# Kernel optimization log

Hardware: AMD Instinct MI355X
Metric: run time of the kernel (lower is better)

The kernel has to match this reference:

```python
import jax, jax.numpy as jnp
import numpy as np

DIM = 1024
D_STATE = 64
D_CONV = 4
EXPAND = 2
D_INNER = DIM * EXPAND          # 2048
N_HEADS = D_INNER // 64         # 32
HEAD_DIM = D_INNER // N_HEADS   # 64
B_SZ = 1
SEQ = 1024
D_IN_PROJ = 2 * D_INNER + 2 * D_STATE + N_HEADS  # 4256
EPS = 1e-6


def setup_inputs() -> dict:
    key = jax.random.key(0)
    ks = jax.random.split(key, 9)
    x = jax.random.normal(ks[0], (B_SZ, SEQ, DIM), jnp.float32)
    W_in = jax.random.normal(ks[1], (D_IN_PROJ, DIM), jnp.float32) / np.sqrt(DIM)
    W_conv = jax.random.normal(ks[2], (D_INNER, 1, D_CONV), jnp.float32) / np.sqrt(D_CONV)
    b_conv = 0.01 * jax.random.normal(ks[3], (D_INNER,), jnp.float32)
    # A_log init: log(arange(1..d_state)) broadcast to (h, d, n), as in the module
    A_log = jnp.log(jnp.arange(1, D_STATE + 1, dtype=jnp.float32)) * jnp.ones((N_HEADS, HEAD_DIM, D_STATE), jnp.float32)
    D = jnp.ones((N_HEADS, HEAD_DIM), jnp.float32) + 0.01 * jax.random.normal(ks[4], (N_HEADS, HEAD_DIM), jnp.float32)
    dt_bias = 0.1 * jax.random.normal(ks[5], (N_HEADS,), jnp.float32)
    norm_w = jnp.ones((D_INNER,), jnp.float32) + 0.01 * jax.random.normal(ks[6], (D_INNER,), jnp.float32)
    W_out = jax.random.normal(ks[7], (DIM, D_INNER), jnp.float32) / np.sqrt(D_INNER)
    return {"x": x, "W_in": W_in, "W_conv": W_conv, "b_conv": b_conv,
            "A_log": A_log, "D": D, "dt_bias": dt_bias, "norm_w": norm_w, "W_out": W_out}


def reference(x, W_in, W_conv, b_conv, A_log, D, dt_bias, norm_w, W_out):
    Bsz, L, _ = x.shape
    zxBCdt = x @ W_in.T  # (B, L, D_IN_PROJ)
    z, xin, Bm, Cm, dt = jnp.split(
        zxBCdt,
        [D_INNER, 2 * D_INNER, 2 * D_INNER + D_STATE, 2 * D_INNER + 2 * D_STATE],
        axis=-1)
    # causal depthwise conv1d (padding d_conv-1 then truncate == left-pad d_conv-1)
    xc = jnp.transpose(xin, (0, 2, 1))  # (B, d_inner, L)
    xc = jax.lax.conv_general_dilated(
        xc, W_conv, window_strides=(1,), padding=[(D_CONV - 1, 0)],
        feature_group_count=D_INNER, dimension_numbers=("NCH", "OIH", "NCH"))
    xc = xc + b_conv[None, :, None]
    xin = jax.nn.silu(jnp.transpose(xc, (0, 2, 1)))  # (B, L, d_inner)
    xh = xin.reshape(Bsz, L, N_HEADS, HEAD_DIM)      # (B, L, h, d)

    A = -jnp.exp(A_log)                     # (h, d, n)
    dt = jax.nn.softplus(dt + dt_bias)      # (B, L, h)

    def step(h_state, ins):
        x_t, dt_t, B_t, C_t = ins  # (B,h,d), (B,h), (B,n), (B,n)
        a = jnp.exp(dt_t[:, :, None, None] * A[None])          # (B,h,d,n)
        h_state = a * h_state + B_t[:, None, None, :] * x_t[..., None]
        y_t = jnp.einsum("bhdn,bn->bhd", h_state, C_t)
        return h_state, y_t

    h0 = jnp.zeros((Bsz, N_HEADS, HEAD_DIM, D_STATE), x.dtype)
    xs = (jnp.moveaxis(xh, 1, 0), jnp.moveaxis(dt, 1, 0),
          jnp.moveaxis(Bm, 1, 0), jnp.moveaxis(Cm, 1, 0))
    _, ys = jax.lax.scan(step, h0, xs)
    y = jnp.moveaxis(ys, 0, 1)              # (B, L, h, d)
    y = y + xh * D[None, None]              # skip term
    y = y.reshape(Bsz, L, D_INNER)
    y = y * jax.nn.silu(z)                  # gating
    rms = jnp.sqrt(jnp.mean(y * y, axis=-1, keepdims=True) + EPS)
    y = y / rms * norm_w                    # RMSNorm
    return y @ W_out.T                      # (B, L, dim)
```

## Files before the change

kernel.cpp:

```cpp
#include <hip/hip_runtime.h>

typedef unsigned short u16;
typedef unsigned int u32;
typedef __attribute__((ext_vector_type(8))) short bf16x8;
typedef __attribute__((ext_vector_type(4))) float f32x4;

#define GPTR(p) ((const __attribute__((address_space(1))) void*)(p))
#define SPTR(p) ((__attribute__((address_space(3))) void*)(p))

#define L_SEQ 1024
#define DIM 1024
#define D_INNER 2048
#define D_STATE 64
#define N_HEADS 32
#define NPROJ 4256
#define NPROJ_PAD 4352
#define COL_Z 0
#define COL_X 2048
#define COL_B 4096
#define COL_C 4160
#define COL_DT 4224
#define NCHUNK 32
#define QCH 32

__device__ __forceinline__ u16 f2bf(float f) {
    unsigned int u = __float_as_uint(f);
    u = u + 0x7fffu + ((u >> 16) & 1u);
    return (u16)(u >> 16);
}
__device__ __forceinline__ float bf2f(u16 h) {
    unsigned int u = ((unsigned int)h) << 16;
    return __uint_as_float(u);
}

__global__ __launch_bounds__(256)
void cast_all_kernel(const float* __restrict__ x, const float* __restrict__ W_in,
                     const float* __restrict__ W_out,
                     u16* __restrict__ xb_hi, u16* __restrict__ xb_lo,
                     u16* __restrict__ Winb, u16* __restrict__ Winb_lo,
                     u16* __restrict__ Woutb)
{
    const int b = blockIdx.x;
    if (b < 1024) {
        const int i = (b * 256 + threadIdx.x) * 4;
        const float4 v = *(const float4*)&x[i];
        const float vs[4] = { v.x, v.y, v.z, v.w };
        u16 oh[4], ol[4];
        #pragma unroll
        for (int j = 0; j < 4; ++j) {
            oh[j] = f2bf(vs[j]);
            ol[j] = f2bf(vs[j] - bf2f(oh[j]));
        }
        *(ushort4*)&xb_hi[i] = *(ushort4*)oh;
        *(ushort4*)&xb_lo[i] = *(ushort4*)ol;
    } else if (b < 5376) {
        const int i = ((b - 1024) * 256 + threadIdx.x) * 4;
        float4 v = make_float4(0.f, 0.f, 0.f, 0.f);
        if (i < NPROJ * DIM) v = *(const float4*)&W_in[i];
        u16 o[4] = { f2bf(v.x), f2bf(v.y), f2bf(v.z), f2bf(v.w) };
        *(ushort4*)&Winb[i] = *(ushort4*)o;
    } else if (b < 5632) {
        const int i = ((b - 5376) * 256 + threadIdx.x) * 4;
        float4 v = make_float4(0.f, 0.f, 0.f, 0.f);
        if (i < (NPROJ - 4096) * DIM) v = *(const float4*)&W_in[(size_t)4096 * DIM + i];
        const float vs[4] = { v.x, v.y, v.z, v.w };
        u16 oh[4], ol[4];
        #pragma unroll
        for (int j = 0; j < 4; ++j) {
            oh[j] = f2bf(vs[j]);
            ol[j] = f2bf(vs[j] - bf2f(oh[j]));
        }
        *(ushort4*)&Winb[(size_t)4096 * DIM + i] = *(ushort4*)oh;
        *(ushort4*)&Winb_lo[i] = *(ushort4*)ol;
    } else {
        const int i = ((b - 5632) * 256 + threadIdx.x) * 4;
        const float4 v = *(const float4*)&W_out[i];
        u16 o[4] = { f2bf(v.x), f2bf(v.y), f2bf(v.z), f2bf(v.w) };
        *(ushort4*)&Woutb[i] = *(ushort4*)o;
    }
}

__global__ __launch_bounds__(256, 2)
void gemm_bt64(const u16* __restrict__ Ah, const u16* __restrict__ Al,
               const u16* __restrict__ Bh, const u16* __restrict__ Bl,
               float* __restrict__ C, int K, int ldc, int precise_from)
{
    __shared__ u16 As[2][64 * 32];
    __shared__ u16 Bs[2][64 * 32];
    __shared__ u16 AsL[2][64 * 32];
    __shared__ u16 BsL[2][64 * 32];
    const int tid  = threadIdx.x;
    const int wave = tid >> 6;
    const int lane = tid & 63;
    const int row0 = blockIdx.y * 64;
    const int col0 = blockIdx.x * 64;
    const int wm = (wave >> 1) * 32;
    const int wn = (wave & 1) * 32;
    const bool precise = ((int)blockIdx.x >= precise_from);

    f32x4 acc[2][2] = {};

    const int r15 = lane & 15;
    const int ko  = (lane >> 4) * 8;

    const int srr = tid >> 2;
    const int skk = (tid & 3) * 8;
    const int lofs = wave * 512;

    auto stage = [&](int buf, int kt) {
        const size_t goff = (size_t)(row0 + srr) * K + kt + skk;
        const size_t gofb = (size_t)(col0 + srr) * K + kt + skk;
        __builtin_amdgcn_global_load_lds(GPTR(Ah + goff), SPTR(&As[buf][lofs]), 16, 0, 0);
        __builtin_amdgcn_global_load_lds(GPTR(Bh + gofb), SPTR(&Bs[buf][lofs]), 16, 0, 0);
        if (precise) {
            __builtin_amdgcn_global_load_lds(GPTR(Al + goff), SPTR(&AsL[buf][lofs]), 16, 0, 0);
            __builtin_amdgcn_global_load_lds(GPTR(Bl + gofb), SPTR(&BsL[buf][lofs]), 16, 0, 0);
        }
    };

    stage(0, 0);
    __syncthreads();
    int cur = 0;
    const int nt = K / 32;
    for (int it = 0; it < nt; ++it) {
        if (it + 1 < nt) stage(cur ^ 1, (it + 1) * 32);
        bf16x8 av[2], bv[2];
        #pragma unroll
        for (int i = 0; i < 2; ++i)
            av[i] = *(const bf16x8*)&As[cur][(wm + i * 16 + r15) * 32 + ko];
        #pragma unroll
        for (int j = 0; j < 2; ++j)
            bv[j] = *(const bf16x8*)&Bs[cur][(wn + j * 16 + r15) * 32 + ko];
        if (precise) {
            bf16x8 avl[2], bvl[2];
            #pragma unroll
            for (int i = 0; i < 2; ++i)
                avl[i] = *(const bf16x8*)&AsL[cur][(wm + i * 16 + r15) * 32 + ko];
            #pragma unroll
            for (int j = 0; j < 2; ++j)
                bvl[j] = *(const bf16x8*)&BsL[cur][(wn + j * 16 + r15) * 32 + ko];
            #pragma unroll
            for (int i = 0; i < 2; ++i)
                #pragma unroll
                for (int j = 0; j < 2; ++j) {
                    acc[i][j] = __builtin_amdgcn_mfma_f32_16x16x32_bf16(av[i],  bv[j],  acc[i][j], 0, 0, 0);
                    acc[i][j] = __builtin_amdgcn_mfma_f32_16x16x32_bf16(av[i],  bvl[j], acc[i][j], 0, 0, 0);
                    acc[i][j] = __builtin_amdgcn_mfma_f32_16x16x32_bf16(avl[i], bv[j],  acc[i][j], 0, 0, 0);
                }
        } else {
            #pragma unroll
            for (int i = 0; i < 2; ++i)
                #pragma unroll
                for (int j = 0; j < 2; ++j)
                    acc[i][j] = __builtin_amdgcn_mfma_f32_16x16x32_bf16(av[i], bv[j], acc[i][j], 0, 0, 0);
        }
        __syncthreads();
        cur ^= 1;
    }

    const int cl = lane & 15;
    const int rg = (lane >> 4) * 4;
    #pragma unroll
    for (int i = 0; i < 2; ++i)
        #pragma unroll
        for (int j = 0; j < 2; ++j)
            #pragma unroll
            for (int reg = 0; reg < 4; ++reg) {
                const int rrow = row0 + wm + i * 16 + rg + reg;
                const int ccol = col0 + wn + j * 16 + cl;
                C[(size_t)rrow * ldc + ccol] = acc[i][j][reg];
            }
}

__global__ __launch_bounds__(256, 2)
void gemm_bt128_sk(const u16* __restrict__ Ah, const u16* __restrict__ Bh,
                   float* __restrict__ Cpart, int Kslice, int lda, int ldb, int ldc)
{
    __shared__ u16 As[2][128 * 32];
    __shared__ u16 Bs[2][128 * 32];
    const int tid  = threadIdx.x;
    const int wave = tid >> 6;
    const int lane = tid & 63;
    const int row0 = blockIdx.y * 128;
    const int col0 = blockIdx.x * 128;
    const int wm = (wave >> 1) * 64;
    const int wn = (wave & 1) * 64;
    const int kbase = blockIdx.z * Kslice;
    float* Cp = Cpart + (size_t)blockIdx.z * (1024 * 1024);

    f32x4 acc[4][4] = {};
    const int r15 = lane & 15;
    const int ko  = (lane >> 4) * 8;

    auto stage = [&](int buf, int kt) {
        #pragma unroll
        for (int call = 0; call < 2; ++call) {
            const int ob = call * 4096 + wave * 1024 + lane * 16;
            const int rr = ob >> 6;
            const int kk = (ob & 63) >> 1;
            const int lofs = call * 2048 + wave * 512;
            __builtin_amdgcn_global_load_lds(GPTR(Ah + (size_t)(row0 + rr) * lda + kt + kk),
                                             SPTR(&As[buf][lofs]), 16, 0, 0);
            __builtin_amdgcn_global_load_lds(GPTR(Bh + (size_t)(col0 + rr) * ldb + kt + kk),
                                             SPTR(&Bs[buf][lofs]), 16, 0, 0);
        }
    };

    stage(0, kbase);
    __syncthreads();
    int cur = 0;
    const int nt = Kslice / 32;
    for (int it = 0; it < nt; ++it) {
        if (it + 1 < nt) stage(cur ^ 1, kbase + (it + 1) * 32);
        bf16x8 av[4], bv[4];
        #pragma unroll
        for (int i = 0; i < 4; ++i)
            av[i] = *(const bf16x8*)&As[cur][(wm + i * 16 + r15) * 32 + ko];
        #pragma unroll
        for (int j = 0; j < 4; ++j)
            bv[j] = *(const bf16x8*)&Bs[cur][(wn + j * 16 + r15) * 32 + ko];
        #pragma unroll
        for (int i = 0; i < 4; ++i)
            #pragma unroll
            for (int j = 0; j < 4; ++j)
                acc[i][j] = __builtin_amdgcn_mfma_f32_16x16x32_bf16(av[i], bv[j], acc[i][j], 0, 0, 0);
        __syncthreads();
        cur ^= 1;
    }

    const int cl = lane & 15;
    const int rg = (lane >> 4) * 4;
    #pragma unroll
    for (int i = 0; i < 4; ++i)
        #pragma unroll
        for (int j = 0; j < 4; ++j)
            #pragma unroll
            for (int reg = 0; reg < 4; ++reg)
                Cp[(size_t)(row0 + wm + i * 16 + rg + reg) * ldc + col0 + wn + j * 16 + cl]
                    = acc[i][j][reg];
}

__global__ __launch_bounds__(256)
void reduce4_kernel(const float* __restrict__ Cpart, float* __restrict__ out)
{
    const int i = (blockIdx.x * 256 + threadIdx.x) * 4;
    const float4 a = *(const float4*)&Cpart[i];
    const float4 b = *(const float4*)&Cpart[i + 1024 * 1024];
    const float4 c = *(const float4*)&Cpart[i + 2 * 1024 * 1024];
    const float4 d = *(const float4*)&Cpart[i + 3 * 1024 * 1024];
    *(float4*)&out[i] = make_float4(a.x + b.x + c.x + d.x, a.y + b.y + c.y + d.y,
                                    a.z + b.z + c.z + d.z, a.w + b.w + c.w + d.w);
}

__global__ __launch_bounds__(256)
void conv_dt_kernel(const float* __restrict__ P,
                    const float* __restrict__ Wc,
                    const float* __restrict__ bc,
                    const float* __restrict__ dtb,
                    const float* __restrict__ A_log,
                    float* __restrict__ xconv,
                    float2* __restrict__ BCp2,
                    float* __restrict__ gT,
                    float* __restrict__ decayT)
{
    const int b = blockIdx.x;
    if (b < 1024) {
        const int t = b;
        const int tid = threadIdx.x;
        const int c0 = tid * 8;
        float acc[8];
        #pragma unroll
        for (int j = 0; j < 8; ++j) acc[j] = bc[c0 + j];
        #pragma unroll
        for (int k = 0; k < 4; ++k) {
            const int tt = t - 3 + k;
            if (tt >= 0) {
                const float* row = P + (size_t)tt * NPROJ_PAD + COL_X + c0;
                float4 a0 = *(const float4*)row;
                float4 a1 = *(const float4*)(row + 4);
                float xv[8] = { a0.x, a0.y, a0.z, a0.w, a1.x, a1.y, a1.z, a1.w };
                #pragma unroll
                for (int j = 0; j < 8; ++j)
                    acc[j] = fmaf(xv[j], Wc[(c0 + j) * 4 + k], acc[j]);
            }
        }
        float o[8];
        #pragma unroll
        for (int j = 0; j < 8; ++j) {
            const float v = acc[j];
            o[j] = v / (1.f + __expf(-v));
        }
        float* dst = xconv + (size_t)t * D_INNER + c0;
        *(float4*)dst       = make_float4(o[0], o[1], o[2], o[3]);
        *(float4*)(dst + 4) = make_float4(o[4], o[5], o[6], o[7]);
        if (tid < 64) {
            const float Bv = P[(size_t)t * NPROJ_PAD + COL_B + tid];
            const float Cv = P[(size_t)t * NPROJ_PAD + COL_C + tid];
            BCp2[t * 64 + tid] = make_float2(Bv, Cv);
        }
    } else {
        const int wv = threadIdx.x >> 6;
        const int lane = threadIdx.x & 63;
        const int idx = (b - 1024) * 4 + wv;
        const int h = idx >> 4;
        const int pr = idx & 15;
        const int t0 = pr * 64;
        float v = P[(size_t)(t0 + lane) * NPROJ_PAD + COL_DT + h] + dtb[h];
        v = (v > 15.f) ? v : __logf(1.f + __expf(v));
        float g = v;
        #pragma unroll
        for (int off = 1; off < 32; off <<= 1) {
            const float u = __shfl_up(g, off);
            if ((lane & 31) >= off) g += u;
        }
        gT[h * L_SEQ + t0 + lane] = g;
        const float Av = -__expf(A_log[(size_t)h * 4096 + lane]);
        #pragma unroll 8
        for (int tt = 0; tt < 64; ++tt) {
            const float dtt = __shfl(v, tt);
            decayT[((size_t)h * L_SEQ + t0 + tt) * 64 + lane] = __expf(dtt * Av);
        }
    }
}

__global__ __launch_bounds__(256)
void xpose_kernel(const float* __restrict__ xconv, float* __restrict__ xT)
{
    __shared__ float tile[64][65];
    const int t0 = blockIdx.x * 64;
    const int c0 = blockIdx.y * 64;
    const int lr = threadIdx.x >> 6;
    const int lc = threadIdx.x & 63;
    #pragma unroll
    for (int r = 0; r < 16; ++r) {
        const int row = r * 4 + lr;
        tile[row][lc] = xconv[(size_t)(t0 + row) * D_INNER + c0 + lc];
    }
    __syncthreads();
    #pragma unroll
    for (int r = 0; r < 16; ++r) {
        const int row = r * 4 + lr;
        xT[(size_t)(c0 + row) * L_SEQ + t0 + lc] = tile[lc][row];
    }
}

__global__ __launch_bounds__(128, 4)
void scan_local_kernel(const float2* __restrict__ BCp2,
                       const float* __restrict__ decayT,
                       const float* __restrict__ xT,
                       float* __restrict__ ygt,
                       u16* __restrict__ S)
{
    __shared__ float2 pt[2][8][2][65];
    const int wv = threadIdx.x >> 6;
    const int lane = threadIdx.x & 63;
    const int hd0 = blockIdx.x * 16 + wv * 8;
    const int pr = blockIdx.y;
    const int h = hd0 >> 6;
    const int tb = pr * 64;

    float sA[8] = {0.f,0.f,0.f,0.f,0.f,0.f,0.f,0.f};
    float sB[8] = {0.f,0.f,0.f,0.f,0.f,0.f,0.f,0.f};

    const float2* bcA = BCp2 + (size_t)tb * 64 + lane;
    const float2* bcB = bcA + 32 * 64;
    const float* dAp = decayT + ((size_t)h * L_SEQ + tb) * 64 + lane;
    const float* dBp = dAp + 32 * 64;
    const float* xr0 = xT + (size_t)hd0 * L_SEQ + tb;

    const int r16 = lane & 15;
    const int seg = lane >> 4;
    const int rd = r16 >> 1;
    const int ri = r16 & 1;

    #pragma unroll
    for (int g = 0; g < 8; ++g) {
        float xA[8][4], xB[8][4];
        #pragma unroll
        for (int d = 0; d < 8; ++d) {
            const float* xr = xr0 + d * L_SEQ;
            const float4 a = *(const float4*)(xr + g * 4);
            const float4 b = *(const float4*)(xr + 32 + g * 4);
            xA[d][0]=a.x; xA[d][1]=a.y; xA[d][2]=a.z; xA[d][3]=a.w;
            xB[d][0]=b.x; xB[d][1]=b.y; xB[d][2]=b.z; xB[d][3]=b.w;
        }
        #pragma unroll
        for (int half = 0; half < 2; ++half) {
            #pragma unroll
            for (int ii2 = 0; ii2 < 2; ++ii2) {
                const int ii = half * 2 + ii2;
                const int i = g * 4 + ii;
                const float2 vA = bcA[i * 64];
                const float2 vB = bcB[i * 64];
                const float aA = dAp[i * 64];
                const float aB = dBp[i * 64];
                #pragma unroll
                for (int d = 0; d < 8; ++d) {
                    sA[d] = fmaf(aA, sA[d], vA.x * xA[d][ii]);
                    sB[d] = fmaf(aB, sB[d], vB.x * xB[d][ii]);
                }
                #pragma unroll
                for (int d = 0; d < 8; ++d)
                    pt[wv][d][ii2][lane] = make_float2(sA[d] * vA.y, sB[d] * vB.y);
            }
            float px = 0.f, py = 0.f;
            #pragma unroll
            for (int k = 0; k < 16; ++k) {
                const float2 v = pt[wv][rd][ri][seg * 16 + k];
                px += v.x; py += v.y;
            }
            px += __shfl_xor(px, 16); py += __shfl_xor(py, 16);
            px += __shfl_xor(px, 32); py += __shfl_xor(py, 32);
            if (lane < 16) {
                const int tA = tb + g * 4 + half * 2 + ri;
                ygt[(size_t)tA * D_INNER + hd0 + rd] = px;
                ygt[(size_t)(tA + 32) * D_INNER + hd0 + rd] = py;
            }
        }
    }
    #pragma unroll
    for (int d = 0; d < 8; ++d) {
        S[((size_t)(hd0 + d) * NCHUNK + pr * 2    ) * 64 + lane] = f2bf(sA[d]);
        S[((size_t)(hd0 + d) * NCHUNK + pr * 2 + 1) * 64 + lane] = f2bf(sB[d]);
    }
}

__global__ __launch_bounds__(256)
void chunk_combine_kernel(const float* __restrict__ A_log,
                          const float* __restrict__ gT,
                          u16* __restrict__ S)
{
    const int tid = blockIdx.x * 256 + threadIdx.x;
    const int hd = tid >> 6;
    const int n  = tid & 63;
    const int h  = hd >> 6;
    const float Av = -__expf(A_log[(size_t)hd * 64 + n]);
    float H = 0.f;
    #pragma unroll 8
    for (int c = 0; c < NCHUNK; ++c) {
        const float Gc = gT[h * L_SEQ + c * QCH + QCH - 1];
        const size_t idx = ((size_t)hd * NCHUNK + c) * 64 + n;
        const float Sl = bf2f(S[idx]);
        S[idx] = f2bf(H);
        H = __expf(Av * Gc) * H + Sl;
    }
}

__global__ __launch_bounds__(256, 2)
void scan_cross_mfma(const float* __restrict__ P,
                     const float* __restrict__ gT,
                     const float* __restrict__ A_log,
                     const u16* __restrict__ S,
                     float* __restrict__ ygt)
{
    const int wv = threadIdx.x >> 6;
    const int lane = threadIdx.x & 63;
    const int idx = blockIdx.x * 4 + wv;
    const int h = idx >> 5;
    const int c = idx & 31;
    const int t0 = c * QCH;
    const int l15 = lane & 15;
    const int lk  = (lane >> 4) * 8;

    float Av8[2][8];
    #pragma unroll
    for (int ss = 0; ss < 2; ++ss)
        #pragma unroll
        for (int qq = 0; qq < 8; ++qq)
            Av8[ss][qq] = -__expf(A_log[(size_t)h * 4096 + ss * 32 + lk + qq]);

    bf16x8 fH[4][2];
    #pragma unroll
    for (int i = 0; i < 4; ++i)
        #pragma unroll
        for (int ss = 0; ss < 2; ++ss)
            fH[i][ss] = *(const bf16x8*)&S[((size_t)(h * 64 + i * 16 + l15) * NCHUNK + c) * 64 + ss * 32 + lk];

    bf16x8 fC[2][2];
    #pragma unroll
    for (int j = 0; j < 2; ++j) {
        const int t = t0 + j * 16 + l15;
        const float g = gT[h * L_SEQ + t];
        #pragma unroll
        for (int ss = 0; ss < 2; ++ss) {
            const float* src = P + (size_t)t * NPROJ_PAD + COL_C + ss * 32 + lk;
            const float4 a = *(const float4*)src;
            const float4 b = *(const float4*)(src + 4);
            const float v[8] = { a.x, a.y, a.z, a.w, b.x, b.y, b.z, b.w };
            bf16x8 rr;
            #pragma unroll
            for (int qq = 0; qq < 8; ++qq)
                rr[qq] = (short)f2bf(v[qq] * __expf(Av8[ss][qq] * g));
            fC[j][ss] = rr;
        }
    }

    f32x4 acc[2][4] = {};
    #pragma unroll
    for (int ss = 0; ss < 2; ++ss)
        #pragma unroll
        for (int j = 0; j < 2; ++j)
            #pragma unroll
            for (int i = 0; i < 4; ++i)
                acc[j][i] = __builtin_amdgcn_mfma_f32_16x16x32_bf16(fC[j][ss], fH[i][ss], acc[j][i], 0, 0, 0);

    const int rg = (lane >> 4) * 4;
    #pragma unroll
    for (int j = 0; j < 2; ++j)
        #pragma unroll
        for (int i = 0; i < 4; ++i)
            #pragma unroll
            for (int rr = 0; rr < 4; ++rr) {
                const int t = t0 + j * 16 + rg + rr;
                const int d = h * 64 + i * 16 + l15;
                ygt[(size_t)t * D_INNER + d] += acc[j][i][rr];
            }
}

__global__ __launch_bounds__(256)
void rmsnorm_kernel(const float* __restrict__ ygt,
                    const float* __restrict__ P,
                    const float* __restrict__ xconv,
                    const float* __restrict__ Dp,
                    const float* __restrict__ nw,
                    u16* __restrict__ Yb)
{
    __shared__ float red[4];
    const int t = blockIdx.x;
    const int tid = threadIdx.x;
    const int c0 = tid * 8;
    const float* zrow = P + (size_t)t * NPROJ_PAD + COL_Z + c0;
    const float4 z0 = *(const float4*)zrow;
    const float4 z1 = *(const float4*)(zrow + 4);
    const float zz[8] = { z0.x, z0.y, z0.z, z0.w, z1.x, z1.y, z1.z, z1.w };
    const float* xrow = xconv + (size_t)t * D_INNER + c0;
    const float4 x0 = *(const float4*)xrow;
    const float4 x1 = *(const float4*)(xrow + 4);
    const float xx[8] = { x0.x, x0.y, x0.z, x0.w, x1.x, x1.y, x1.z, x1.w };
    const float4 d0 = *(const float4*)&Dp[c0];
    const float4 d1 = *(const float4*)&Dp[c0 + 4];
    const float dd[8] = { d0.x, d0.y, d0.z, d0.w, d1.x, d1.y, d1.z, d1.w };
    const float* yrow = ygt + (size_t)t * D_INNER + c0;
    const float4 y0 = *(const float4*)yrow;
    const float4 y1 = *(const float4*)(yrow + 4);
    const float yy[8] = { y0.x, y0.y, y0.z, y0.w, y1.x, y1.y, y1.z, y1.w };
    float v[8];
    float ss = 0.f;
    #pragma unroll
    for (int j = 0; j < 8; ++j) {
        const float yv = yy[j] + dd[j] * xx[j];
        const float z = zz[j];
        const float gated = yv * (z / (1.f + __expf(-z)));
        v[j] = gated;
        ss += gated * gated;
    }
    #pragma unroll
    for (int off = 32; off > 0; off >>= 1) ss += __shfl_xor(ss, off);
    const int wave = tid >> 6;
    if ((tid & 63) == 0) red[wave] = ss;
    __syncthreads();
    const float total = red[0] + red[1] + red[2] + red[3];
    const float scale = rsqrtf(total * (1.f / D_INNER) + 1e-6f);
    u16 o[8];
    #pragma unroll
    for (int j = 0; j < 8; ++j)
        o[j] = f2bf(v[j] * scale * nw[c0 + j]);
    *(uint4*)&Yb[(size_t)t * D_INNER + c0] = *(uint4*)o;
}

extern "C" void kernel_launch(void* const* d_in, const int* in_sizes, int n_in,
                              void* d_out, int out_size, void* d_ws, size_t ws_size,
                              hipStream_t stream)
{
    const float* x      = (const float*)d_in[0];
    const float* W_in   = (const float*)d_in[1];
    const float* W_conv = (const float*)d_in[2];
    const float* b_conv = (const float*)d_in[3];
    const float* A_log  = (const float*)d_in[4];
    const float* Dp     = (const float*)d_in[5];
    const float* dt_bias= (const float*)d_in[6];
    const float* norm_w = (const float*)d_in[7];
    const float* W_out  = (const float*)d_in[8];
    float* out = (float*)d_out;

    char* w = (char*)d_ws;
    u16*   xb_hi  = (u16*)(w);
    u16*   xb_lo  = (u16*)(w + (2u  << 20));
    u16*   Winb   = (u16*)(w + (4u  << 20));
    u16*   Winb_lo= (u16*)(w + (12u << 20) + (512u << 10));
    float* decayT = (float*)(w);
    u16*   Yb     = (u16*)(w);
    u16*   S      = (u16*)(w + (8u  << 20));
    u16*   Woutb  = (u16*)(w + (16u << 20));
    float* P      = (float*)(w + (20u << 20));
    float* Cpart  = (float*)(w + (20u << 20));
    float* xconv  = (float*)(w + (37u << 20));
    float* gT     = (float*)(w + (45u << 20));
    float2* BCp2  = (float2*)(w + (45u << 20) + (512u << 10));
    float* ygt    = (float*)(w + (46u << 20));
    float* xT     = (float*)(w + (54u << 20));

    const u16* Winb_lo_virt = Winb_lo - (size_t)4096 * DIM;

    cast_all_kernel<<<dim3(7680), 256, 0, stream>>>(
        x, W_in, W_out, xb_hi, xb_lo, Winb, Winb_lo, Woutb);

    gemm_bt64<<<dim3(NPROJ_PAD / 64, L_SEQ / 64), 256, 0, stream>>>(
        xb_hi, xb_lo, Winb, Winb_lo_virt, P, DIM, NPROJ_PAD, 64);

    conv_dt_kernel<<<dim3(1024 + 128), 256, 0, stream>>>(
        P, W_conv, b_conv, dt_bias, A_log, xconv, BCp2, gT, decayT);

    xpose_kernel<<<dim3(L_SEQ / 64, D_INNER / 64), 256, 0, stream>>>(xconv, xT);

    scan_local_kernel<<<dim3(D_INNER / 16, 16), 128, 0, stream>>>(
        BCp2, decayT, xT, ygt, S);
    chunk_combine_kernel<<<dim3(D_INNER * 64 / 256), 256, 0, stream>>>(A_log, gT, S);
    scan_cross_mfma<<<dim3(N_HEADS * NCHUNK / 4), 256, 0, stream>>>(P, gT, A_log, S, ygt);

    rmsnorm_kernel<<<dim3(L_SEQ), 256, 0, stream>>>(ygt, P, xconv, Dp, norm_w, Yb);

    gemm_bt128_sk<<<dim3(DIM / 128, L_SEQ / 128, 4), 256, 0, stream>>>(
        Yb, Woutb, Cpart, D_INNER / 4, D_INNER, D_INNER, DIM);
    reduce4_kernel<<<dim3(DIM * L_SEQ / 4 / 256), 256, 0, stream>>>(Cpart, out);
}
```

Measured before the change: 150.0 us.

## Use K=64 tiles with XOR-swizzled LDS and serialize hi/lo split-precision passes

The bf16 GEMM now stages 64-wide K tiles instead of 32-wide ones and applies an XOR swizzle to the LDS layout, which targets bank conflicts on the MFMA operand reads. The separate low-part LDS buffers are removed. For precise blocks, the three hi/lo product terms run as separate sequential stage/compute iterations that reuse the same buffers. This halves the number of barriers per K for non-precise blocks and cuts LDS usage, but precise blocks now reload the hi tiles several times and need more synchronizations.

```diff
diff --git a/kernel.cpp b/kernel.cpp
--- a/kernel.cpp
+++ b/kernel.cpp
@@ -85,10 +85,8 @@
                const u16* __restrict__ Bh, const u16* __restrict__ Bl,
                float* __restrict__ C, int K, int ldc, int precise_from)
 {
-    __shared__ u16 As[2][64 * 32];
-    __shared__ u16 Bs[2][64 * 32];
-    __shared__ u16 AsL[2][64 * 32];
-    __shared__ u16 BsL[2][64 * 32];
+    __shared__ u16 As[2][64 * 64];
+    __shared__ u16 Bs[2][64 * 64];
     const int tid  = threadIdx.x;
     const int wave = tid >> 6;
     const int lane = tid & 63;
@@ -101,53 +99,51 @@
     f32x4 acc[2][2] = {};
 
     const int r15 = lane & 15;
-    const int ko  = (lane >> 4) * 8;
-
-    const int srr = tid >> 2;
-    const int skk = (tid & 3) * 8;
-    const int lofs = wave * 512;
-
-    auto stage = [&](int buf, int kt) {
-        const size_t goff = (size_t)(row0 + srr) * K + kt + skk;
-        const size_t gofb = (size_t)(col0 + srr) * K + kt + skk;
-        __builtin_amdgcn_global_load_lds(GPTR(Ah + goff), SPTR(&As[buf][lofs]), 16, 0, 0);
-        __builtin_amdgcn_global_load_lds(GPTR(Bh + gofb), SPTR(&Bs[buf][lofs]), 16, 0, 0);
-        if (precise) {
-            __builtin_amdgcn_global_load_lds(GPTR(Al + goff), SPTR(&AsL[buf][lofs]), 16, 0, 0);
-            __builtin_amdgcn_global_load_lds(GPTR(Bl + gofb), SPTR(&BsL[buf][lofs]), 16, 0, 0);
+    const int q4  = lane >> 4;
+
+    const int reps = precise ? 3 : 1;
+    const int nt = K / 64;
+    const int total = nt * reps;
+
+    auto stage = [&](int buf, int it) {
+        const int kt = (it / reps) * 64;
+        const int sub = it - (it / reps) * reps;
+        const u16* Asrc = (sub == 2) ? Al : Ah;
+        const u16* Bsrc = (sub == 1) ? Bl : Bh;
+        #pragma unroll
+        for (int call = 0; call < 2; ++call) {
+            const int ob = call * 4096 + tid * 16;
+            const int row = ob >> 7;
+            const int chk = (ob >> 4) & 7;
+            const int sch = chk ^ (row & 7);
+            const int gk = kt + sch * 8;
+            const int lofs = (call * 4096 + wave * 1024) >> 1;
+            __builtin_amdgcn_global_load_lds(GPTR(Asrc + (size_t)(row0 + row) * K + gk),
+                                             SPTR(&As[buf][lofs]), 16, 0, 0);
+            __builtin_amdgcn_global_load_lds(GPTR(Bsrc + (size_t)(col0 + row) * K + gk),
+                                             SPTR(&Bs[buf][lofs]), 16, 0, 0);
         }
     };
 
     stage(0, 0);
     __syncthreads();
     int cur = 0;
-    const int nt = K / 32;
-    for (int it = 0; it < nt; ++it) {
-        if (it + 1 < nt) stage(cur ^ 1, (it + 1) * 32);
-        bf16x8 av[2], bv[2];
-        #pragma unroll
-        for (int i = 0; i < 2; ++i)
-            av[i] = *(const bf16x8*)&As[cur][(wm + i * 16 + r15) * 32 + ko];
-        #pragma unroll
-        for (int j = 0; j < 2; ++j)
-            bv[j] = *(const bf16x8*)&Bs[cur][(wn + j * 16 + r15) * 32 + ko];
-        if (precise) {
-            bf16x8 avl[2], bvl[2];
-            #pragma unroll
-            for (int i = 0; i < 2; ++i)
-                avl[i] = *(const bf16x8*)&AsL[cur][(wm + i * 16 + r15) * 32 + ko];
-            #pragma unroll
-            for (int j = 0; j < 2; ++j)
-                bvl[j] = *(const bf16x8*)&BsL[cur][(wn + j * 16 + r15) * 32 + ko];
-            #pragma unroll
-            for (int i = 0; i < 2; ++i)
-                #pragma unroll
-                for (int j = 0; j < 2; ++j) {
-                    acc[i][j] = __builtin_amdgcn_mfma_f32_16x16x32_bf16(av[i],  bv[j],  acc[i][j], 0, 0, 0);
-                    acc[i][j] = __builtin_amdgcn_mfma_f32_16x16x32_bf16(av[i],  bvl[j], acc[i][j], 0, 0, 0);
-                    acc[i][j] = __builtin_amdgcn_mfma_f32_16x16x32_bf16(avl[i], bv[j],  acc[i][j], 0, 0, 0);
-                }
-        } else {
+    for (int it = 0; it < total; ++it) {
+        if (it + 1 < total) stage(cur ^ 1, it + 1);
+        #pragma unroll
+        for (int s = 0; s < 2; ++s) {
+            const int cbase = s * 4 + q4;
+            bf16x8 av[2], bv[2];
+            #pragma unroll
+            for (int i = 0; i < 2; ++i) {
+                const int r = wm + i * 16 + r15;
+                av[i] = *(const bf16x8*)&As[cur][r * 64 + ((cbase ^ (r & 7)) * 8)];
+            }
+            #pragma unroll
+            for (int j = 0; j < 2; ++j) {
+                const int r = wn + j * 16 + r15;
+                bv[j] = *(const bf16x8*)&Bs[cur][r * 64 + ((cbase ^ (r & 7)) * 8)];
+            }
             #pragma unroll
             for (int i = 0; i < 2; ++i)
                 #pragma unroll
```

New measurement: 144.3 us. 1.04x faster.
